# Kernel optimization log

Measured on AMD Instinct MI355X. Metric: run time of the kernel, lower is better.

Reference implementation:

```python
import jax, jax.numpy as jnp
import numpy as np

N_NODES = 100000
N_EDGES = 1600000
MUL = 32            # channel multiplicity for every irrep
INV_SQRT_MUL = 1.0 / np.sqrt(32.0)
# path constants: wigner-3j norms (1/sqrt3 for 0x1->1 and 1x1->0, 1/sqrt6 for 1x1->1)
# combined with fan-in path normalization (fan=32 for 0e out, fan=64 for 1o out, 2 paths)
C_DOT = 1.0 / np.sqrt(3.0 * 32.0)
C_SCL = 1.0 / np.sqrt(3.0 * 64.0)
C_CRS = 1.0 / np.sqrt(6.0 * 64.0)


def setup_inputs() -> dict:
    key = jax.random.key(0)
    ks = jax.random.split(key, 12)
    x = jax.random.normal(ks[0], (N_NODES, 128), jnp.float32)
    pos = jax.random.normal(ks[1], (N_NODES, 3), jnp.float32)
    edge_index = jax.random.randint(ks[2], (2, N_EDGES), 0, N_NODES, jnp.int32)
    # o3.Linear(32x0e+32x1o -> 32x0e+32x0e+32x1o): per-irrep channel mixing
    W_node_s = jax.random.normal(ks[3], (32, 64), jnp.float32)   # 0e -> (scalars|gates)
    W_node_v = jax.random.normal(ks[4], (32, 32), jnp.float32)   # 1o -> 1o
    # FullyConnectedTensorProduct(32x0e+32x1o, 1x1o -> 32x0e+32x1o): 3 CG paths
    W_tp_d = jax.random.normal(ks[5], (32, 32), jnp.float32)     # 1o x 1o -> 0e (dot)
    W_tp_s = jax.random.normal(ks[6], (32, 32), jnp.float32)     # 0e x 1o -> 1o
    W_tp_c = jax.random.normal(ks[7], (32, 32), jnp.float32)     # 1o x 1o -> 1o (cross)
    # o3.Linear(32x0e+32x1o -> 32x0e+32x1o)
    W_msg_s = jax.random.normal(ks[8], (32, 32), jnp.float32)
    W_msg_v = jax.random.normal(ks[9], (32, 32), jnp.float32)
    ln_gamma = jnp.ones((128,), jnp.float32)
    ln_beta = jnp.zeros((128,), jnp.float32)
    return {"x": x, "pos": pos, "edge_index": edge_index,
            "W_node_s": W_node_s, "W_node_v": W_node_v,
            "W_tp_d": W_tp_d, "W_tp_s": W_tp_s, "W_tp_c": W_tp_c,
            "W_msg_s": W_msg_s, "W_msg_v": W_msg_v,
            "ln_gamma": ln_gamma, "ln_beta": ln_beta}


def reference(x, pos, edge_index, W_node_s, W_node_v, W_tp_d, W_tp_s, W_tp_c,
              W_msg_s, W_msg_v, ln_gamma, ln_beta):
    N = x.shape[0]
    row, col = edge_index[0], edge_index[1]
    # split node irreps: 32 scalars (0e) | 32 vectors (1o) of dim 3
    s = x[:, :32]                       # [N,32]
    v = x[:, 32:].reshape(-1, 32, 3)    # [N,32,3]
    # lin_node (equivariant linear, path-normalized by 1/sqrt(fan_in)=1/sqrt(32))
    h_s = (s @ W_node_s) * INV_SQRT_MUL                          # [N,64]
    h_v = jnp.einsum('nid,ij->njd', v, W_node_v) * INV_SQRT_MUL  # [N,32,3]
    # Gate: relu scalars, sigmoid gates multiply the gated vectors
    sc = jax.nn.relu(h_s[:, :32])                                # [N,32]
    hv = h_v * jax.nn.sigmoid(h_s[:, 32:])[:, :, None]           # [N,32,3]
    # spherical harmonics l=1, component norm: sqrt(3)*unit vec in e3nn (y,z,x) order
    rel = pos[col] - pos[row]                                    # [E,3]
    unit = rel / jnp.sqrt(jnp.sum(rel * rel, -1, keepdims=True) + 1e-12)
    u = jnp.sqrt(3.0) * unit[:, (1, 2, 0)]                       # [E,3]
    # gather source-node features per edge
    sj = sc[col]                                                 # [E,32]
    vj = hv[col]                                                 # [E,32,3]
    # CG tensor product paths
    dot = jnp.einsum('eid,ed->ei', vj, u)                        # 1o x 1o -> 0e
    crs = jnp.cross(vj, u[:, None, :])                           # 1o x 1o -> 1o
    m0 = (dot @ W_tp_d) * C_DOT                                  # [E,32]
    m1 = (sj @ W_tp_s)[:, :, None] * u[:, None, :] * C_SCL \
         + jnp.einsum('eid,ik->ekd', crs, W_tp_c) * C_CRS        # [E,32,3]
    m = jnp.concatenate([m0, m1.reshape(-1, 96)], -1)            # [E,128]
    # scatter-mean over destination nodes (row)
    deg = jax.ops.segment_sum(jnp.ones_like(row, jnp.float32), row,
                              num_segments=N).clip(1.0)
    mi = jax.ops.segment_sum(m, row, num_segments=N) / deg[:, None]
    # lin_msg
    ms = (mi[:, :32] @ W_msg_s) * INV_SQRT_MUL
    mv = jnp.einsum('nid,ij->njd', mi[:, 32:].reshape(-1, 32, 3),
                    W_msg_v) * INV_SQRT_MUL
    o = jnp.concatenate([ms, mv.reshape(-1, 96)], -1)            # [N,128]
    # LayerNorm over 128 dims (as in the original, affine)
    mu = o.mean(-1, keepdims=True)
    var = o.var(-1, keepdims=True)
    o = (o - mu) / jnp.sqrt(var + 1e-5) * ln_gamma + ln_beta
    return x + o
```

## Files before the change

kernel.cpp:

```cpp
#include <hip/hip_runtime.h>
#include <math.h>


static constexpr float INV_SQRT_MUL = 0.17677669529663687f;
static constexpr float C_DOT = 0.10206207261596575f;
static constexpr float C_SCL = 0.07216878364870322f;
static constexpr float C_CRS = 0.05103103630798288f;
static constexpr float SQRT3 = 1.7320508075688772f;
static constexpr int MAXDEG = 48;
static constexpr int PH1_B = 1024;

#define WS_ALIGN(x) (((x) + 255) & ~(size_t)255)

__device__ __forceinline__ unsigned short f2bf(float v) {
    unsigned int b = __float_as_uint(v);
    b += 0x7FFFu + ((b >> 16) & 1u);
    return (unsigned short)(b >> 16);
}
__device__ __forceinline__ float bf2f(unsigned short u) {
    return __uint_as_float(((unsigned int)u) << 16);
}

__global__ __launch_bounds__(1024)
void fuse_zero(const float* __restrict__ Wtpd, const float* __restrict__ Wtps,
               const float* __restrict__ Wtpc, const float* __restrict__ Wms,
               const float* __restrict__ Wmv, float* __restrict__ Wall,
               int* __restrict__ cnt, int N) {
    int t = threadIdx.x;
    if (blockIdx.x == 0) {
        int i = t >> 5, j = t & 31;
        float a = 0.f, b = 0.f, c = 0.f;
#pragma unroll
        for (int k = 0; k < 32; ++k) {
            a += Wtpd[i * 32 + k] * Wms[k * 32 + j];
            b += Wtps[i * 32 + k] * Wmv[k * 32 + j];
            c += Wtpc[i * 32 + k] * Wmv[k * 32 + j];
        }
        Wall[t]        = a * (C_DOT * INV_SQRT_MUL);
        Wall[1024 + t] = b * (C_SCL * INV_SQRT_MUL);
        Wall[2048 + t] = c * (C_CRS * INV_SQRT_MUL);
    } else {
        int i = (blockIdx.x - 1) * 1024 + t;
        if (i < N) cnt[i] = 0;
    }
}

__global__ __launch_bounds__(256)
void phase1(const float* __restrict__ x, const float* __restrict__ Wns,
            const float* __restrict__ Wnv, const int* __restrict__ eidx,
            ushort4* __restrict__ feat4, int* __restrict__ cnt,
            int* __restrict__ slots, int N, int E) {
    __shared__ float xs[2 * 128];
    int t = threadIdx.x;
    if (t < 128) {
        int tid = blockIdx.x * 128 + t;
        const int stride = PH1_B * 128;
        int Q = E >> 2;
        const int4* r4p = (const int4*)eidx;
        const int4* c4p = (const int4*)(eidx + E);
        for (int q = tid; q < Q; q += stride) {
            int4 R = r4p[q];
            int4 C = c4p[q];
            int rr[4] = {R.x, R.y, R.z, R.w};
            int cc[4] = {C.x, C.y, C.z, C.w};
            int p[4];
#pragma unroll
            for (int k = 0; k < 4; ++k) p[k] = atomicAdd(&cnt[rr[k]], 1);
#pragma unroll
            for (int k = 0; k < 4; ++k)
                if (p[k] < MAXDEG) slots[(size_t)rr[k] * MAXDEG + p[k]] = cc[k];
        }
        for (int e = (Q << 2) + tid; e < E; e += stride) {
            int r = eidx[e], c = eidx[E + e];
            int p = atomicAdd(&cnt[r], 1);
            if (p < MAXDEG) slots[(size_t)r * MAXDEG + p] = c;
        }
    } else {
        int wv2 = (t >> 6) - 2;
        int lane = t & 63;
        int i = lane & 31;
        float w[32], wg[32];
        if (lane < 32) {
#pragma unroll
            for (int k = 0; k < 32; ++k) w[k] = Wns[k * 64 + i];
        } else {
#pragma unroll
            for (int k = 0; k < 32; ++k) { w[k] = Wnv[k * 32 + i]; wg[k] = Wns[k * 64 + 32 + i]; }
        }
        float* xw = xs + wv2 * 128;
        const float4* xw4 = (const float4*)xw;
        const float2* x2 = (const float2*)x;
        int wid = blockIdx.x * 2 + wv2;
        const int stride = PH1_B * 2;

        int n = wid;
        float2 cur = make_float2(0.f, 0.f);
        if (n < N) cur = x2[(size_t)n * 64 + lane];
        while (n < N) {
            int n2 = n + stride;
            float2 nxt = make_float2(0.f, 0.f);
            if (n2 < N) nxt = x2[(size_t)n2 * 64 + lane];
            ((float2*)xw)[lane] = cur;

            float outS = 0.f, o0 = 0.f, o1 = 0.f, o2 = 0.f;
            if (lane < 32) {
                float h = 0.f;
#pragma unroll
                for (int j = 0; j < 8; ++j) {
                    float4 q = xw4[j];
                    h += q.x * w[4*j] + q.y * w[4*j+1] + q.z * w[4*j+2] + q.w * w[4*j+3];
                }
                outS = fmaxf(h * INV_SQRT_MUL, 0.f);
            } else {
                float gs = 0.f;
#pragma unroll
                for (int j = 0; j < 8; ++j) {
                    float4 q = xw4[j];
                    gs += q.x * wg[4*j] + q.y * wg[4*j+1] + q.z * wg[4*j+2] + q.w * wg[4*j+3];
                }
#pragma unroll
                for (int j = 0; j < 24; ++j) {
                    float4 q = xw4[8 + j];
                    float vals[4] = {q.x, q.y, q.z, q.w};
#pragma unroll
                    for (int m = 0; m < 4; ++m) {
                        int e = 4 * j + m;
                        int k = e / 3, d = e % 3;
                        float f = vals[m] * w[k];
                        if (d == 0) o0 += f; else if (d == 1) o1 += f; else o2 += f;
                    }
                }
                float sig = 1.f / (1.f + expf(-gs * INV_SQRT_MUL));
                float sc = INV_SQRT_MUL * sig;
                o0 *= sc; o1 *= sc; o2 *= sc;
            }
            float scv = __shfl(outS, i);
            if (lane >= 32) {
                ushort4 pk;
                pk.x = f2bf(scv); pk.y = f2bf(o0); pk.z = f2bf(o1); pk.w = f2bf(o2);
                feat4[(size_t)n * 32 + i] = pk;
            }
            cur = nxt; n = n2;
        }
    }
}

template <int U>
__device__ __forceinline__ void agg_chunk(const float4* __restrict__ curow, int j,
    const ushort4* __restrict__ feat4, int lane,
    float& D, float& S0, float& S1, float& S2,
    float& C0, float& C1, float& C2) {
    float4 q[U];
    ushort4 f[U];
#pragma unroll
    for (int k = 0; k < U; ++k) q[k] = curow[j + k];
#pragma unroll
    for (int k = 0; k < U; ++k)
        f[k] = feat4[(size_t)__float_as_int(q[k].w) * 32 + lane];
#pragma unroll
    for (int k = 0; k < U; ++k) {
        float u0 = q[k].x, u1 = q[k].y, u2 = q[k].z;
        float sj = bf2f(f[k].x);
        float h0 = bf2f(f[k].y), h1 = bf2f(f[k].z), h2 = bf2f(f[k].w);
        D  += h0 * u0 + h1 * u1 + h2 * u2;
        S0 += sj * u0; S1 += sj * u1; S2 += sj * u2;
        C0 += h1 * u2 - h2 * u1;
        C1 += h2 * u0 - h0 * u2;
        C2 += h0 * u1 - h1 * u0;
    }
}

__global__ __launch_bounds__(256)
void agg(const float* __restrict__ x, const float* __restrict__ pos,
         const ushort4* __restrict__ feat4, const int* __restrict__ cnt,
         const int* __restrict__ slots, const float* __restrict__ Wall,
         const float* __restrict__ gamma, const float* __restrict__ beta,
         float* __restrict__ out, int N) {
    int t = threadIdx.x;
    int hw = t >> 5, lane = t & 31;
    int n = blockIdx.x * 8 + hw;
    bool live = (n < N);
    int nn = live ? n : 0;

    __shared__ float4 cu[8][MAXDEG];
    __shared__ float4 finA[8][32];
    __shared__ float4 finB[8][32];

    int deg = live ? cnt[n] : 0;
    int c = min(deg, MAXDEG);

    float prx = pos[nn * 3 + 0], pry = pos[nn * 3 + 1], prz = pos[nn * 3 + 2];

    if (lane < c) {
        int col = slots[(size_t)nn * MAXDEG + lane];
        float rx = pos[col * 3 + 0] - prx, ry = pos[col * 3 + 1] - pry, rz = pos[col * 3 + 2] - prz;
        float inv = rsqrtf(rx * rx + ry * ry + rz * rz + 1e-12f) * SQRT3;
        cu[hw][lane] = make_float4(ry * inv, rz * inv, rx * inv, __int_as_float(col));
    }
    if (lane + 32 < c) {
        int col = slots[(size_t)nn * MAXDEG + 32 + lane];
        float rx = pos[col * 3 + 0] - prx, ry = pos[col * 3 + 1] - pry, rz = pos[col * 3 + 2] - prz;
        float inv = rsqrtf(rx * rx + ry * ry + rz * rz + 1e-12f) * SQRT3;
        cu[hw][32 + lane] = make_float4(ry * inv, rz * inv, rx * inv, __int_as_float(col));
    }
    __syncthreads();

    float D = 0.f, S0 = 0.f, S1 = 0.f, S2 = 0.f, C0 = 0.f, C1 = 0.f, C2 = 0.f;
    const float4* curow = cu[hw];
    int j = 0;
    for (; j + 8 <= c; j += 8) agg_chunk<8>(curow, j, feat4, lane, D, S0, S1, S2, C0, C1, C2);
    if (j + 4 <= c) { agg_chunk<4>(curow, j, feat4, lane, D, S0, S1, S2, C0, C1, C2); j += 4; }
    for (; j < c; ++j) agg_chunk<1>(curow, j, feat4, lane, D, S0, S1, S2, C0, C1, C2);

    finA[hw][lane] = make_float4(D, S0, S1, S2);
    finB[hw][lane] = make_float4(C0, C1, C2, 0.f);
    __syncthreads();

    float invdeg = 1.0f / (float)((deg > 0) ? deg : 1);
    float a0 = 0.f, aV0 = 0.f, aV1 = 0.f, aV2 = 0.f;
#pragma unroll 8
    for (int i = 0; i < 32; ++i) {
        float4 a = finA[hw][i];
        float4 b = finB[hw][i];
        float wd = Wall[i * 32 + lane];
        float ws = Wall[1024 + i * 32 + lane];
        float wc = Wall[2048 + i * 32 + lane];
        a0  += a.x * wd;
        aV0 += a.y * ws + b.x * wc;
        aV1 += a.z * ws + b.y * wc;
        aV2 += a.w * ws + b.z * wc;
    }
    float vd = a0 * invdeg;
    float v0 = aV0 * invdeg, v1 = aV1 * invdeg, v2 = aV2 * invdeg;

    float s1 = vd + v0 + v1 + v2;
    float s2 = vd * vd + v0 * v0 + v1 * v1 + v2 * v2;
#pragma unroll
    for (int m = 16; m >= 1; m >>= 1) {
        s1 += __shfl_xor(s1, m);
        s2 += __shfl_xor(s2, m);
    }
    float mu = s1 * (1.f / 128.f);
    float var = s2 * (1.f / 128.f) - mu * mu;
    float rstd = rsqrtf(var + 1e-5f);

    if (live) {
        size_t base = (size_t)n * 128;
        int chv = 32 + lane * 3;
        float xv0 = __builtin_nontemporal_load(&x[base + lane]);
        float xa  = __builtin_nontemporal_load(&x[base + chv + 0]);
        float xb  = __builtin_nontemporal_load(&x[base + chv + 1]);
        float xc  = __builtin_nontemporal_load(&x[base + chv + 2]);
        __builtin_nontemporal_store(xv0 + (vd - mu) * rstd * gamma[lane] + beta[lane], &out[base + lane]);
        __builtin_nontemporal_store(xa + (v0 - mu) * rstd * gamma[chv + 0] + beta[chv + 0], &out[base + chv + 0]);
        __builtin_nontemporal_store(xb + (v1 - mu) * rstd * gamma[chv + 1] + beta[chv + 1], &out[base + chv + 1]);
        __builtin_nontemporal_store(xc + (v2 - mu) * rstd * gamma[chv + 2] + beta[chv + 2], &out[base + chv + 2]);
    }
}

extern "C" void kernel_launch(void* const* d_in, const int* in_sizes, int n_in,
                              void* d_out, int out_size, void* d_ws, size_t ws_size,
                              hipStream_t stream) {
    const float* x     = (const float*)d_in[0];
    const float* pos   = (const float*)d_in[1];
    const int*   eidx  = (const int*)d_in[2];
    const float* Wns   = (const float*)d_in[3];
    const float* Wnv   = (const float*)d_in[4];
    const float* Wtpd  = (const float*)d_in[5];
    const float* Wtps  = (const float*)d_in[6];
    const float* Wtpc  = (const float*)d_in[7];
    const float* Wms   = (const float*)d_in[8];
    const float* Wmv   = (const float*)d_in[9];
    const float* gamma = (const float*)d_in[10];
    const float* beta  = (const float*)d_in[11];
    float* out = (float*)d_out;

    int N = in_sizes[0] / 128;
    int E = in_sizes[2] / 2;

    char* ws = (char*)d_ws;
    size_t off = 0;
    unsigned short* feat = (unsigned short*)(ws + off); off += WS_ALIGN((size_t)N * 128 * 2);
    int*   cnt  = (int*)(ws + off);   off += WS_ALIGN((size_t)N * 4);
    float* Wall = (float*)(ws + off); off += WS_ALIGN(3072 * 4);
    int*   slots = (int*)(ws + off);

    int zb = 1 + (N + 1023) / 1024;
    fuse_zero<<<zb, 1024, 0, stream>>>(Wtpd, Wtps, Wtpc, Wms, Wmv, Wall, cnt, N);
    phase1<<<PH1_B, 256, 0, stream>>>(x, Wns, Wnv, eidx, (ushort4*)feat, cnt, slots, N, E);
    agg<<<(N + 7) / 8, 256, 0, stream>>>(x, pos, (const ushort4*)feat, cnt, slots, Wall, gamma, beta, out, N);
}
```

Before: 434.7 us.

## Split phase1 into sharded edge scatter and thread-per-node feature kernel

Replaces the combined phase1 kernel with two kernels. The first is an edge scatter sharded by row&7, with the counters relaid out so each shard's atomics fall in a contiguous region (CIDX). The second is a node_feat kernel in which each thread computes one node's linear layer from an LDS-staged tile, reading transposed weights precomputed in fuse_zero. The aim is better atomic locality across L2/XCDs and higher compute parallelism for the node linear. In exchange, every shard rereads the row array eight times, the node kernel holds a large register footprint of 96+32 floats, and it launches only 64-thread blocks. The counter array is fixed at 8*16384 words, which assumes N is at most 131072.

New measurement: 437.5 us. About the same (+0.6%).

```diff
diff --git a/kernel.cpp b/kernel.cpp
--- a/kernel.cpp
+++ b/kernel.cpp
@@ -8,9 +8,11 @@
 static constexpr float C_CRS = 0.05103103630798288f;
 static constexpr float SQRT3 = 1.7320508075688772f;
 static constexpr int MAXDEG = 48;
-static constexpr int PH1_B = 1024;
+static constexpr int SCAT_B = 2048;
+static constexpr int CNT_WORDS = 8 * 16384;
 
 #define WS_ALIGN(x) (((x) + 255) & ~(size_t)255)
+#define CIDX(r) ((((r) & 7) << 14) | ((r) >> 3))
 
 __device__ __forceinline__ unsigned short f2bf(float v) {
     unsigned int b = __float_as_uint(v);
@@ -22,10 +24,11 @@
 }
 
 __global__ __launch_bounds__(1024)
-void fuse_zero(const float* __restrict__ Wtpd, const float* __restrict__ Wtps,
+void fuse_zero(const float* __restrict__ Wns, const float* __restrict__ Wnv,
+               const float* __restrict__ Wtpd, const float* __restrict__ Wtps,
                const float* __restrict__ Wtpc, const float* __restrict__ Wms,
                const float* __restrict__ Wmv, float* __restrict__ Wall,
-               int* __restrict__ cnt, int N) {
+               int* __restrict__ cnt) {
     int t = threadIdx.x;
     if (blockIdx.x == 0) {
         int i = t >> 5, j = t & 31;
@@ -39,109 +42,143 @@
         Wall[t]        = a * (C_DOT * INV_SQRT_MUL);
         Wall[1024 + t] = b * (C_SCL * INV_SQRT_MUL);
         Wall[2048 + t] = c * (C_CRS * INV_SQRT_MUL);
+        int i2 = t >> 5, k2 = t & 31;
+        Wall[3072 + t]        = Wns[k2 * 64 + i2];
+        Wall[3072 + 1024 + t] = Wns[k2 * 64 + 32 + i2];
+        Wall[5120 + t]        = Wnv[k2 * 32 + i2];
     } else {
         int i = (blockIdx.x - 1) * 1024 + t;
-        if (i < N) cnt[i] = 0;
+        if (i < CNT_WORDS) cnt[i] = 0;
     }
 }
 
 __global__ __launch_bounds__(256)
-void phase1(const float* __restrict__ x, const float* __restrict__ Wns,
-            const float* __restrict__ Wnv, const int* __restrict__ eidx,
-            ushort4* __restrict__ feat4, int* __restrict__ cnt,
-            int* __restrict__ slots, int N, int E) {
-    __shared__ float xs[2 * 128];
-    int t = threadIdx.x;
-    if (t < 128) {
-        int tid = blockIdx.x * 128 + t;
-        const int stride = PH1_B * 128;
-        int Q = E >> 2;
-        const int4* r4p = (const int4*)eidx;
-        const int4* c4p = (const int4*)(eidx + E);
-        for (int q = tid; q < Q; q += stride) {
-            int4 R = r4p[q];
-            int4 C = c4p[q];
-            int rr[4] = {R.x, R.y, R.z, R.w};
-            int cc[4] = {C.x, C.y, C.z, C.w};
-            int p[4];
-#pragma unroll
-            for (int k = 0; k < 4; ++k) p[k] = atomicAdd(&cnt[rr[k]], 1);
-#pragma unroll
-            for (int k = 0; k < 4; ++k)
-                if (p[k] < MAXDEG) slots[(size_t)rr[k] * MAXDEG + p[k]] = cc[k];
-        }
-        for (int e = (Q << 2) + tid; e < E; e += stride) {
-            int r = eidx[e], c = eidx[E + e];
-            int p = atomicAdd(&cnt[r], 1);
+void scatter(const int* __restrict__ eidx, int* __restrict__ cnt,
+             int* __restrict__ slots, int E) {
+    int shard = blockIdx.x & 7;
+    int tid = (blockIdx.x >> 3) * 256 + threadIdx.x;
+    const int SSTRIDE = (SCAT_B / 8) * 256;
+    int Q = E >> 2;
+    const int4* r4p = (const int4*)eidx;
+    const int4* c4p = (const int4*)(eidx + E);
+    for (int q = tid; q < Q; q += SSTRIDE) {
+        int4 R = r4p[q];
+        bool any = ((R.x & 7) == shard) | ((R.y & 7) == shard) |
+                   ((R.z & 7) == shard) | ((R.w & 7) == shard);
+        if (!any) continue;
+        int4 C = c4p[q];
+        int rr[4] = {R.x, R.y, R.z, R.w};
+        int cc[4] = {C.x, C.y, C.z, C.w};
+#pragma unroll
+        for (int k = 0; k < 4; ++k) {
+            if ((rr[k] & 7) == shard) {
+                int p = atomicAdd(&cnt[CIDX(rr[k])], 1);
+                if (p < MAXDEG) slots[(size_t)rr[k] * MAXDEG + p] = cc[k];
+            }
+        }
+    }
+    for (int e = (Q << 2) + tid; e < E; e += SSTRIDE) {
+        int r = eidx[e];
+        if ((r & 7) == shard) {
+            int c = eidx[E + e];
+            int p = atomicAdd(&cnt[CIDX(r)], 1);
             if (p < MAXDEG) slots[(size_t)r * MAXDEG + p] = c;
         }
-    } else {
-        int wv2 = (t >> 6) - 2;
-        int lane = t & 63;
-        int i = lane & 31;
-        float w[32], wg[32];
-        if (lane < 32) {
-#pragma unroll
-            for (int k = 0; k < 32; ++k) w[k] = Wns[k * 64 + i];
-        } else {
-#pragma unroll
-            for (int k = 0; k < 32; ++k) { w[k] = Wnv[k * 32 + i]; wg[k] = Wns[k * 64 + 32 + i]; }
-        }
-        float* xw = xs + wv2 * 128;
-        const float4* xw4 = (const float4*)xw;
-        const float2* x2 = (const float2*)x;
-        int wid = blockIdx.x * 2 + wv2;
-        const int stride = PH1_B * 2;
-
-        int n = wid;
-        float2 cur = make_float2(0.f, 0.f);
-        if (n < N) cur = x2[(size_t)n * 64 + lane];
-        while (n < N) {
-            int n2 = n + stride;
-            float2 nxt = make_float2(0.f, 0.f);
-            if (n2 < N) nxt = x2[(size_t)n2 * 64 + lane];
-            ((float2*)xw)[lane] = cur;
-
-            float outS = 0.f, o0 = 0.f, o1 = 0.f, o2 = 0.f;
-            if (lane < 32) {
-                float h = 0.f;
-#pragma unroll
-                for (int j = 0; j < 8; ++j) {
-                    float4 q = xw4[j];
-                    h += q.x * w[4*j] + q.y * w[4*j+1] + q.z * w[4*j+2] + q.w * w[4*j+3];
-                }
-                outS = fmaxf(h * INV_SQRT_MUL, 0.f);
-            } else {
-                float gs = 0.f;
-#pragma unroll
-                for (int j = 0; j < 8; ++j) {
-                    float4 q = xw4[j];
-                    gs += q.x * wg[4*j] + q.y * wg[4*j+1] + q.z * wg[4*j+2] + q.w * wg[4*j+3];
-                }
-#pragma unroll
-                for (int j = 0; j < 24; ++j) {
-                    float4 q = xw4[8 + j];
-                    float vals[4] = {q.x, q.y, q.z, q.w};
-#pragma unroll
-                    for (int m = 0; m < 4; ++m) {
-                        int e = 4 * j + m;
-                        int k = e / 3, d = e % 3;
-                        float f = vals[m] * w[k];
-                        if (d == 0) o0 += f; else if (d == 1) o1 += f; else o2 += f;
-                    }
-                }
-                float sig = 1.f / (1.f + expf(-gs * INV_SQRT_MUL));
-                float sc = INV_SQRT_MUL * sig;
-                o0 *= sc; o1 *= sc; o2 *= sc;
-            }
-            float scv = __shfl(outS, i);
-            if (lane >= 32) {
-                ushort4 pk;
-                pk.x = f2bf(scv); pk.y = f2bf(o0); pk.z = f2bf(o1); pk.w = f2bf(o2);
-                feat4[(size_t)n * 32 + i] = pk;
-            }
-            cur = nxt; n = n2;
-        }
+    }
+}
+
+__global__ __launch_bounds__(64)
+void node_feat(const float* __restrict__ x, const float* __restrict__ WT,
+               ushort4* __restrict__ feat4, int N) {
+    __shared__ float buf[64 * 100];
+    int l = threadIdx.x;
+    int nt = (N + 63) >> 6;
+    const float* WnsT = WT;
+    const float* WnvT = WT + 2048;
+    for (int tile = blockIdx.x; tile < nt; tile += gridDim.x) {
+        int B = tile << 6;
+        {
+            int r0 = l >> 3, cw = (l & 7) * 4;
+            for (int j = 0; j < 8; ++j) {
+                int row = j * 8 + r0;
+                int node = B + row;
+                float4 v = make_float4(0.f, 0.f, 0.f, 0.f);
+                if (node < N) v = *(const float4*)(x + (size_t)node * 128 + cw);
+                *(float4*)(buf + row * 36 + cw) = v;
+            }
+        }
+        __syncthreads();
+        float xsv[32];
+        {
+            const float4* rp = (const float4*)(buf + l * 36);
+#pragma unroll
+            for (int j = 0; j < 8; ++j) {
+                float4 q = rp[j];
+                xsv[4 * j] = q.x; xsv[4 * j + 1] = q.y;
+                xsv[4 * j + 2] = q.z; xsv[4 * j + 3] = q.w;
+            }
+        }
+        unsigned int scp[16];
+        float sig[32];
+#pragma unroll 2
+        for (int i = 0; i < 32; ++i) {
+            float a = 0.f, g = 0.f;
+#pragma unroll
+            for (int k = 0; k < 32; ++k) {
+                a += xsv[k] * WnsT[i * 32 + k];
+                g += xsv[k] * WnsT[(32 + i) * 32 + k];
+            }
+            a = fmaxf(a * INV_SQRT_MUL, 0.f);
+            float s = 1.f / (1.f + __expf(-g * INV_SQRT_MUL));
+            unsigned short s16 = f2bf(a);
+            if ((i & 1) == 0) scp[i >> 1] = s16;
+            else scp[i >> 1] |= ((unsigned int)s16) << 16;
+            sig[i] = s * INV_SQRT_MUL;
+        }
+        __syncthreads();
+        {
+            int r0 = l >> 3, cw = (l & 7) * 4;
+            for (int j = 0; j < 24; ++j) {
+                int third = j >> 3, j8 = j & 7;
+                int row = j8 * 8 + r0;
+                int node = B + row;
+                int w0 = 32 + third * 32 + cw;
+                float4 v = make_float4(0.f, 0.f, 0.f, 0.f);
+                if (node < N) v = *(const float4*)(x + (size_t)node * 128 + w0);
+                *(float4*)(buf + row * 100 + (w0 - 32)) = v;
+            }
+        }
+        __syncthreads();
+        float xv[96];
+        {
+            const float4* rp = (const float4*)(buf + l * 100);
+#pragma unroll
+            for (int j = 0; j < 24; ++j) {
+                float4 q = rp[j];
+                xv[4 * j] = q.x; xv[4 * j + 1] = q.y;
+                xv[4 * j + 2] = q.z; xv[4 * j + 3] = q.w;
+            }
+        }
+        int node = B + l;
+        bool live = (node < N);
+#pragma unroll 2
+        for (int i = 0; i < 32; ++i) {
+            float o0 = 0.f, o1 = 0.f, o2 = 0.f;
+#pragma unroll
+            for (int k = 0; k < 32; ++k) {
+                float wv = WnvT[i * 32 + k];
+                o0 += xv[3 * k + 0] * wv;
+                o1 += xv[3 * k + 1] * wv;
+                o2 += xv[3 * k + 2] * wv;
+            }
+            float s = sig[i];
+            unsigned int scw = scp[i >> 1];
+            ushort4 pk;
+            pk.x = (unsigned short)((i & 1) ? (scw >> 16) : (scw & 0xFFFFu));
+            pk.y = f2bf(o0 * s); pk.z = f2bf(o1 * s); pk.w = f2bf(o2 * s);
+            if (live) feat4[(size_t)node * 32 + i] = pk;
+        }
+        __syncthreads();
     }
 }
 
@@ -186,7 +223,7 @@
     __shared__ float4 finA[8][32];
     __shared__ float4 finB[8][32];
 
-    int deg = live ? cnt[n] : 0;
+    int deg = live ? cnt[CIDX(n)] : 0;
     int c = min(deg, MAXDEG);
 
     float prx = pos[nn * 3 + 0], pry = pos[nn * 3 + 1], prz = pos[nn * 3 + 2];
@@ -281,12 +318,14 @@
     char* ws = (char*)d_ws;
     size_t off = 0;
     unsigned short* feat = (unsigned short*)(ws + off); off += WS_ALIGN((size_t)N * 128 * 2);
-    int*   cnt  = (int*)(ws + off);   off += WS_ALIGN((size_t)N * 4);
-    float* Wall = (float*)(ws + off); off += WS_ALIGN(3072 * 4);
+    int*   cnt  = (int*)(ws + off);   off += WS_ALIGN((size_t)CNT_WORDS * 4);
+    float* Wall = (float*)(ws + off); off += WS_ALIGN(6144 * 4);
     int*   slots = (int*)(ws + off);
 
-    int zb = 1 + (N + 1023) / 1024;
-    fuse_zero<<<zb, 1024, 0, stream>>>(Wtpd, Wtps, Wtpc, Wms, Wmv, Wall, cnt, N);
-    phase1<<<PH1_B, 256, 0, stream>>>(x, Wns, Wnv, eidx, (ushort4*)feat, cnt, slots, N, E);
+    int zb = 1 + (CNT_WORDS + 1023) / 1024;
+    fuse_zero<<<zb, 1024, 0, stream>>>(Wns, Wnv, Wtpd, Wtps, Wtpc, Wms, Wmv, Wall, cnt);
+    scatter<<<SCAT_B, 256, 0, stream>>>(eidx, cnt, slots, E);
+    int nt = (N + 63) >> 6;
+    node_feat<<<nt, 64, 0, stream>>>(x, Wall + 3072, (ushort4*)feat, N);
     agg<<<(N + 7) / 8, 256, 0, stream>>>(x, pos, (const ushort4*)feat, cnt, slots, Wall, gamma, beta, out, N);
 }
```
